# Performance work log

Hardware: AMD Instinct MI355X
Metric: run time of the kernel (lower is better)

Reference implementation:

```python
import jax, jax.numpy as jnp
import numpy as np

NUM_QUBITS = 512
NUM_CORES = 16
CORE_SIZE = 64
HIDDEN = 128
BATCH = 2048


def setup_inputs() -> dict:
    key = jax.random.key(0)
    k1, k2, k3 = jax.random.split(key, 3)
    last_assignment = jax.random.randint(k1, (BATCH, NUM_QUBITS), 0, NUM_CORES, dtype=jnp.int32)
    adjacency = jnp.ones((NUM_CORES, NUM_CORES), dtype=jnp.float32)  # all-to-all core graph
    qubit_embedding = jax.random.normal(k2, (NUM_QUBITS + 1, HIDDEN), dtype=jnp.float32)
    gcn_weight = jax.random.normal(k3, (HIDDEN, HIDDEN), dtype=jnp.float32) * (1.0 / np.sqrt(HIDDEN))
    gcn_bias = jnp.zeros((HIDDEN,), dtype=jnp.float32)
    return {
        'last_assignment': last_assignment,
        'adjacency': adjacency,
        'qubit_embedding': qubit_embedding,
        'gcn_weight': gcn_weight,
        'gcn_bias': gcn_bias,
    }


def reference(last_assignment, adjacency, qubit_embedding, gcn_weight, gcn_bias):
    B, Q = last_assignment.shape
    C = adjacency.shape[0]
    # --- replace the sequential per-qubit scatter loop with a single cumsum ---
    # pos[b,q] = number of earlier qubits assigned to the same core (the loop's
    # running counter idx); core index C (the extra row) always writes slot 0
    # because the loop resets its counter every iteration.
    oh = jax.nn.one_hot(last_assignment, C + 1, dtype=jnp.int32)        # [B,Q,C+1]
    cnt = jnp.cumsum(oh, axis=1)                                        # inclusive counts
    pos = jnp.take_along_axis(cnt, last_assignment[..., None], axis=2)[..., 0] - 1
    pos = jnp.where(last_assignment == C, 0, pos)
    buf = jnp.full((B, C + 1, CORE_SIZE), Q, dtype=jnp.int32)           # padding id = num_qubits
    b_idx = jnp.arange(B)[:, None]
    q_idx = jnp.broadcast_to(jnp.arange(Q, dtype=jnp.int32)[None, :], (B, Q))
    buf = buf.at[b_idx, last_assignment, pos].set(q_idx, mode='drop')
    buf = buf[:, :C, :]                                                 # drop overflow core row
    # --- embedding (padding row forced to zero, as nn.Embedding padding_idx) ---
    tbl = qubit_embedding.at[Q].set(0.0)
    qubit_embs = tbl[buf]                                               # [B,C,core_size,H]
    core_embs = qubit_embs.max(axis=2)                                  # [B,C,H]
    # --- GCNConv(add_self_loops=False): D^{-1/2} A D^{-1/2} (X W^T) + b ---
    deg = adjacency.sum(axis=0)
    dinv = jnp.where(deg > 0, 1.0 / jnp.sqrt(deg), 0.0)
    a_norm = adjacency * dinv[:, None] * dinv[None, :]                  # symmetric norm
    h = jnp.einsum('bch,oh->bco', core_embs, gcn_weight)                # lin (PyG: x @ W^T)
    out = jnp.einsum('ij,bjo->bio', a_norm, h) + gcn_bias               # [B,C,H]
    return out
```

## Files before the change

### kernel.cpp

```cpp
#include <hip/hip_runtime.h>
#include <stdint.h>

typedef unsigned short u16;
typedef unsigned int u32;
typedef unsigned long long u64;

typedef __bf16 bf16x8 __attribute__((ext_vector_type(8)));
typedef float f32x4 __attribute__((ext_vector_type(4)));
typedef u16 u16x8 __attribute__((ext_vector_type(8)));

#define NQ 512
#define NC 16
#define NH 128
#define NB 2048
#define QE_KEYS (513*128)
#define WT_OFF  QE_KEYS
#define GW_ELEMS (128*128)
#define A_OFF (WT_OFF + GW_ELEMS)
#define LSEG 1088
#define ESEG 2304
#define ESTRIDE 136

static __device__ __forceinline__ u16 f2bf_rne(float f){
  u32 u = __float_as_uint(f);
  u += 0x7fffu + ((u>>16)&1u);
  return (u16)(u>>16);
}
static __device__ __forceinline__ u32 pack_rne(float lo, float hi){
  return (u32)f2bf_rne(lo) | ((u32)f2bf_rne(hi)<<16);
}
static __device__ __forceinline__ u16 key_of(float f){
  u16 b = f2bf_rne(f);
  return (b & 0x8000u) ? (u16)~b : (u16)(b | 0x8000u);
}
static __device__ __forceinline__ u16 unkey(u16 k){
  return (k & 0x8000u) ? (u16)(k ^ 0x8000u) : (u16)~k;
}

union Frag { u32 u[4]; uint4 u4; bf16x8 f; };
union U8   { u16x8 v; int w[4]; uint4 u4; u16 h[8]; };

__global__ void prepass_kernel(const float* __restrict__ qe,
                               const float* __restrict__ gw,
                               const float* __restrict__ adj,
                               u16* __restrict__ ws)
{
  if (blockIdx.x == 0) {
    __shared__ float sD[16];
    int t = threadIdx.x;
    if (t < 16) {
      float s = 0.f;
      for (int i = 0; i < 16; ++i) s += adj[i*16 + t];
      sD[t] = (s > 0.f) ? (1.0f / sqrtf(s)) : 0.f;
    }
    __syncthreads();
    int i = t >> 4, jp = (t & 15) * 2;
    float lo = (jp   < 16) ? adj[i*16 + jp]   * sD[i] * sD[jp]   : 0.f;
    float hi = (jp+1 < 16) ? adj[i*16 + jp+1] * sD[i] * sD[jp+1] : 0.f;
    ((u32*)(ws + A_OFF))[t] = pack_rne(lo, hi);
    return;
  }
  int idx = (blockIdx.x - 1) * 256 + threadIdx.x;
  if (idx < QE_KEYS/8) {
    int i8 = idx * 8;
    uint4 o;
    if (i8 >= 512*NH) {
      o.x = 0x80008000u; o.y = 0x80008000u; o.z = 0x80008000u; o.w = 0x80008000u;
    } else {
      const float4* p = (const float4*)(qe + i8);
      float4 a = p[0], b = p[1];
      o.x = (u32)key_of(a.x) | ((u32)key_of(a.y)<<16);
      o.y = (u32)key_of(a.z) | ((u32)key_of(a.w)<<16);
      o.z = (u32)key_of(b.x) | ((u32)key_of(b.y)<<16);
      o.w = (u32)key_of(b.z) | ((u32)key_of(b.w)<<16);
    }
    *(uint4*)(ws + i8) = o;
  } else if (idx < QE_KEYS/8 + GW_ELEMS/8) {
    int j8 = (idx - QE_KEYS/8) * 8;
    const float4* p = (const float4*)(gw + j8);
    float4 a = p[0], b = p[1];
    uint4 o;
    o.x = pack_rne(a.x, a.y); o.y = pack_rne(a.z, a.w);
    o.z = pack_rne(b.x, b.y); o.w = pack_rne(b.z, b.w);
    *(uint4*)(ws + WT_OFF + j8) = o;
  }
}

static __device__ __forceinline__ void wave_reduce_max(U8& A){
  U8 B;
  #pragma unroll
  for (int j = 0; j < 4; ++j) B.w[j] = __shfl_xor(A.w[j], 16);
  A.v = __builtin_elementwise_max(A.v, B.v);
  #pragma unroll
  for (int j = 0; j < 4; ++j) B.w[j] = __shfl_xor(A.w[j], 32);
  A.v = __builtin_elementwise_max(A.v, B.v);
}

__global__ __launch_bounds__(256, 4)
void core_snapshot_kernel(const int* __restrict__ la,
                          const u16* __restrict__ ws,
                          const float* __restrict__ gb,
                          float* __restrict__ outp)
{
  __shared__ __align__(16) u16 sListAll[4*LSEG];
  __shared__ __align__(16) u16 sEAll[4*ESEG];

  const int tid  = threadIdx.x;
  const int lane = tid & 63;
  const int wv   = tid >> 6;
  const int m    = lane & 15;
  const int quad = lane >> 4;
  const int item = blockIdx.x*4 + wv;
  u16* sList = sListAll + wv*LSEG;
  u16* sE    = sEAll    + wv*ESEG;
  const u16* qt = ws;
  const u16* wt = ws + WT_OFF;

  {
    uint4 f = make_uint4(0x02000200u,0x02000200u,0x02000200u,0x02000200u);
    *(uint4*)&sList[lane*16]     = f;
    *(uint4*)&sList[lane*16 + 8] = f;
  }

  int av[8];
  #pragma unroll
  for (int ch = 0; ch < 8; ++ch) av[ch] = la[item*NQ + ch*64 + lane];
  const u64 lmask = (1ull << lane) - 1ull;
  u32 runbase = 0;
  #pragma unroll
  for (int ch = 0; ch < 8; ++ch) {
    u32 cnt = 0, intra = 0;
    #pragma unroll
    for (int c = 0; c < 16; ++c) {
      u64 mk = __ballot(av[ch] == c);
      if (lane == c)    cnt   = (u32)__popcll(mk);
      if (av[ch] == c)  intra = (u32)__popcll(mk & lmask);
    }
    u32 base = (u32)__shfl((int)runbase, av[ch]);
    u32 rank = base + intra;
    if (rank < 64) sList[av[ch]*64 + (rank&3)*16 + (rank>>2)] = (u16)(ch*64 + lane);
    runbase += cnt;
  }
  const u32 cntv = runbase;

  const u16* qb = qt + m*8;
  for (int c = 0; c < 16; ++c) {
    int cnt = __shfl((int)cntv, c);
    U8 S0, S1;
    S0.u4 = *(const uint4*)&sList[c*64 + quad*16];
    S1.u4 = *(const uint4*)&sList[c*64 + quad*16 + 8];
    U8 A; A.v = (u16x8)0;
    {
      U8 T[8];
      #pragma unroll
      for (int k = 0; k < 8; ++k) T[k].u4 = *(const uint4*)(qb + (int)S0.h[k]*NH);
      #pragma unroll
      for (int k = 0; k < 8; ++k) A.v = __builtin_elementwise_max(A.v, T[k].v);
    }
    if (cnt > 32) {
      U8 T[8];
      #pragma unroll
      for (int k = 0; k < 8; ++k) T[k].u4 = *(const uint4*)(qb + (int)S1.h[k]*NH);
      #pragma unroll
      for (int k = 0; k < 8; ++k) A.v = __builtin_elementwise_max(A.v, T[k].v);
    }
    wave_reduce_max(A);
    if (cnt < 64) {
      U8 Z; Z.v = (u16x8)(u16)0x8000u;
      A.v = __builtin_elementwise_max(A.v, Z.v);
    }
    if (quad == 0) {
      uint4 e;
      e.x = (u32)unkey(A.h[0]) | ((u32)unkey(A.h[1])<<16);
      e.y = (u32)unkey(A.h[2]) | ((u32)unkey(A.h[3])<<16);
      e.z = (u32)unkey(A.h[4]) | ((u32)unkey(A.h[5])<<16);
      e.w = (u32)unkey(A.h[6]) | ((u32)unkey(A.h[7])<<16);
      *(uint4*)&sE[c*ESTRIDE + m*8] = e;
    }
  }

  bf16x8 af[4];
  #pragma unroll
  for (int ks = 0; ks < 4; ++ks)
    af[ks] = *(const bf16x8*)&sE[m*ESTRIDE + ks*32 + quad*8];
  Frag anf;
  anf.u4 = *(const uint4*)(ws + A_OFF + m*32 + quad*8);

  #pragma unroll
  for (int t = 0; t < 8; ++t) {
    f32x4 acc = {0.f, 0.f, 0.f, 0.f};
    #pragma unroll
    for (int ks = 0; ks < 4; ++ks) {
      bf16x8 bfr = *(const bf16x8*)(wt + (t*16 + m)*NH + ks*32 + quad*8);
      acc = __builtin_amdgcn_mfma_f32_16x16x32_bf16(af[ks], bfr, acc, 0, 0, 0);
    }
    float d16[4], d32[4], lo[4], hi[4];
    #pragma unroll
    for (int r = 0; r < 4; ++r) {
      d16[r] = __shfl_down(acc[r], 16);
      d32[r] = __shfl_down(acc[r], 32);
    }
    #pragma unroll
    for (int r = 0; r < 4; ++r) {
      lo[r] = (quad == 0) ? acc[r] : d16[r];
      hi[r] = (quad == 0) ? d16[r] : d32[r];
    }
    Frag hb;
    hb.u[0] = pack_rne(lo[0], lo[1]); hb.u[1] = pack_rne(lo[2], lo[3]);
    hb.u[2] = pack_rne(hi[0], hi[1]); hb.u[3] = pack_rne(hi[2], hi[3]);
    if (quad >= 2) { hb.u[0]=0; hb.u[1]=0; hb.u[2]=0; hb.u[3]=0; }
    float biasv = gb[t*16 + m];
    f32x4 o4 = {biasv, biasv, biasv, biasv};
    o4 = __builtin_amdgcn_mfma_f32_16x16x32_bf16(anf.f, hb.f, o4, 0, 0, 0);
    float* op = outp + item*(NC*NH) + t*16 + m;
    #pragma unroll
    for (int r = 0; r < 4; ++r) op[(quad*4 + r)*NH] = o4[r];
  }
}

extern "C" void kernel_launch(void* const* d_in, const int* in_sizes, int n_in,
                              void* d_out, int out_size, void* d_ws, size_t ws_size,
                              hipStream_t stream) {
  const int*   la  = (const int*)d_in[0];
  const float* adj = (const float*)d_in[1];
  const float* qe  = (const float*)d_in[2];
  const float* gw  = (const float*)d_in[3];
  const float* gb  = (const float*)d_in[4];
  float* outp = (float*)d_out;
  u16* ws = (u16*)d_ws;

  int pre_blocks = 1 + (QE_KEYS/8 + GW_ELEMS/8 + 255)/256;
  prepass_kernel<<<pre_blocks, 256, 0, stream>>>(qe, gw, adj, ws);
  core_snapshot_kernel<<<NB/4, 256, 0, stream>>>(la, ws, gb, outp);
}
```

Measured before the change: 92.74 us.

## Gather embeddings with 8-byte loads split across half-waves and branchless packed unkey

Reorganizes the per-core max gather so that each lane covers 4 hidden dims and each half-wave takes alternating list slots. Loads drop from 16 bytes to 8 bytes, and the cross-lane reduction needs one shuffle stage instead of two. The slot list becomes linear, and the loads are batched with count-dependent guards in steps of 8, so fewer padding rows are fetched when a core holds between 32 and 64 qubits. The unkey step becomes a branchless packed 32-bit operation. In exchange, each lane issues more, narrower loads, which changes memory coalescing and instruction count.

Measured after the change: 96.29 us. +3.8%, slower.

```diff
diff --git a/kernel.cpp b/kernel.cpp
--- a/kernel.cpp
+++ b/kernel.cpp
@@ -7,7 +7,7 @@
 
 typedef __bf16 bf16x8 __attribute__((ext_vector_type(8)));
 typedef float f32x4 __attribute__((ext_vector_type(4)));
-typedef u16 u16x8 __attribute__((ext_vector_type(8)));
+typedef u16 u16x2 __attribute__((ext_vector_type(2)));
 
 #define NQ 512
 #define NC 16
@@ -33,12 +33,19 @@
   u16 b = f2bf_rne(f);
   return (b & 0x8000u) ? (u16)~b : (u16)(b | 0x8000u);
 }
-static __device__ __forceinline__ u16 unkey(u16 k){
-  return (k & 0x8000u) ? (u16)(k ^ 0x8000u) : (u16)~k;
+static __device__ __forceinline__ u32 pkmax(u32 a, u32 b){
+  union { u32 s; u16x2 v; } A, B, R;
+  A.s = a; B.s = b;
+  R.v = __builtin_elementwise_max(A.v, B.v);
+  return R.s;
+}
+static __device__ __forceinline__ u32 unkey_pk(u32 x){
+  u32 sel = x & 0x80008000u;
+  sel = sel | (sel - (sel >> 15));
+  return (sel & (x ^ 0x80008000u)) | (~sel & ~x);
 }
 
 union Frag { u32 u[4]; uint4 u4; bf16x8 f; };
-union U8   { u16x8 v; int w[4]; uint4 u4; u16 h[8]; };
 
 __global__ void prepass_kernel(const float* __restrict__ qe,
                                const float* __restrict__ gw,
@@ -86,16 +93,6 @@
   }
 }
 
-static __device__ __forceinline__ void wave_reduce_max(U8& A){
-  U8 B;
-  #pragma unroll
-  for (int j = 0; j < 4; ++j) B.w[j] = __shfl_xor(A.w[j], 16);
-  A.v = __builtin_elementwise_max(A.v, B.v);
-  #pragma unroll
-  for (int j = 0; j < 4; ++j) B.w[j] = __shfl_xor(A.w[j], 32);
-  A.v = __builtin_elementwise_max(A.v, B.v);
-}
-
 __global__ __launch_bounds__(256, 4)
 void core_snapshot_kernel(const int* __restrict__ la,
                           const u16* __restrict__ ws,
@@ -110,6 +107,9 @@
   const int wv   = tid >> 6;
   const int m    = lane & 15;
   const int quad = lane >> 4;
+  const int half = lane >> 5;
+  const int dimo = lane & 31;
+  const int sh   = half * 16;
   const int item = blockIdx.x*4 + wv;
   u16* sList = sListAll + wv*LSEG;
   u16* sE    = sEAll    + wv*ESEG;
@@ -138,46 +138,44 @@
     }
     u32 base = (u32)__shfl((int)runbase, av[ch]);
     u32 rank = base + intra;
-    if (rank < 64) sList[av[ch]*64 + (rank&3)*16 + (rank>>2)] = (u16)(ch*64 + lane);
+    if (rank < 64) sList[av[ch]*64 + rank] = (u16)(ch*64 + lane);
     runbase += cnt;
   }
   const u32 cntv = runbase;
 
-  const u16* qb = qt + m*8;
+  const u16* qrow = qt + dimo*4;
+  #define GBATCH(E0, N) { \
+    u32 wd[N]; uint2 T[N]; \
+    _Pragma("unroll") for (int k2 = 0; k2 < N/4; ++k2) { \
+      uint4 W = *(const uint4*)&sList[c*64 + (E0) + k2*8]; \
+      wd[k2*4+0]=W.x; wd[k2*4+1]=W.y; wd[k2*4+2]=W.z; wd[k2*4+3]=W.w; } \
+    _Pragma("unroll") for (int k = 0; k < N; ++k) { \
+      int id = (int)((wd[k] >> sh) & 0xffffu); \
+      T[k] = *(const uint2*)(qrow + id*NH); } \
+    _Pragma("unroll") for (int k = 0; k < N; ++k) { \
+      ax = pkmax(ax, T[k].x); ay = pkmax(ay, T[k].y); } }
+
   for (int c = 0; c < 16; ++c) {
-    int cnt = __shfl((int)cntv, c);
-    U8 S0, S1;
-    S0.u4 = *(const uint4*)&sList[c*64 + quad*16];
-    S1.u4 = *(const uint4*)&sList[c*64 + quad*16 + 8];
-    U8 A; A.v = (u16x8)0;
-    {
-      U8 T[8];
-      #pragma unroll
-      for (int k = 0; k < 8; ++k) T[k].u4 = *(const uint4*)(qb + (int)S0.h[k]*NH);
-      #pragma unroll
-      for (int k = 0; k < 8; ++k) A.v = __builtin_elementwise_max(A.v, T[k].v);
-    }
-    if (cnt > 32) {
-      U8 T[8];
-      #pragma unroll
-      for (int k = 0; k < 8; ++k) T[k].u4 = *(const uint4*)(qb + (int)S1.h[k]*NH);
-      #pragma unroll
-      for (int k = 0; k < 8; ++k) A.v = __builtin_elementwise_max(A.v, T[k].v);
-    }
-    wave_reduce_max(A);
-    if (cnt < 64) {
-      U8 Z; Z.v = (u16x8)(u16)0x8000u;
-      A.v = __builtin_elementwise_max(A.v, Z.v);
-    }
-    if (quad == 0) {
-      uint4 e;
-      e.x = (u32)unkey(A.h[0]) | ((u32)unkey(A.h[1])<<16);
-      e.y = (u32)unkey(A.h[2]) | ((u32)unkey(A.h[3])<<16);
-      e.z = (u32)unkey(A.h[4]) | ((u32)unkey(A.h[5])<<16);
-      e.w = (u32)unkey(A.h[6]) | ((u32)unkey(A.h[7])<<16);
-      *(uint4*)&sE[c*ESTRIDE + m*8] = e;
-    }
-  }
+    int cmin = __builtin_amdgcn_readlane((int)cntv, c);
+    cmin = (cmin > 64) ? 64 : cmin;
+    u32 ax = 0, ay = 0;
+    GBATCH(0, 8)
+    GBATCH(16, 8)
+    if (cmin > 32) GBATCH(32, 4)
+    if (cmin > 40) GBATCH(40, 4)
+    if (cmin > 48) GBATCH(48, 4)
+    if (cmin > 56) GBATCH(56, 4)
+    ax = pkmax(ax, (u32)__shfl_xor((int)ax, 32));
+    ay = pkmax(ay, (u32)__shfl_xor((int)ay, 32));
+    if (cmin < 64) {
+      ax = pkmax(ax, 0x80008000u);
+      ay = pkmax(ay, 0x80008000u);
+    }
+    u32 ex = unkey_pk(ax), ey = unkey_pk(ay);
+    if (half == 0)
+      *(uint2*)&sE[c*ESTRIDE + dimo*4] = make_uint2(ex, ey);
+  }
+  #undef GBATCH
 
   bf16x8 af[4];
   #pragma unroll
```
